# Kernel tuning notes

Measured on AMD Instinct MI355X. Metric: run time of the kernel, lower is better.

The kernel has to match this reference:

```python
import jax, jax.numpy as jnp
import numpy as np

H = 64        # index_n_heads
D = 128       # index_head_dim
R = 64        # rope_head_dim
TOPK = 512    # index_topk
FP8_MAX = 448.0
EPS = 1e-6
THETA = 10000.0


def setup_inputs() -> dict:
    key = jax.random.key(0)
    ks = jax.random.split(key, 6)
    T, DM, QL = 1536, 7168, 1536
    return {
        "hidden_states": jax.random.normal(ks[0], (T, DM), jnp.float32),
        "q_lora": jax.random.normal(ks[1], (T, QL), jnp.float32),
        "wq_b": jax.random.normal(ks[2], (QL, H * D), jnp.float32) / np.sqrt(QL),
        "wk": jax.random.normal(ks[3], (DM, D), jnp.float32) / np.sqrt(DM),
        "k_norm_w": jnp.ones((D,), jnp.float32),
        "k_norm_b": jnp.zeros((D,), jnp.float32),
        "weights_proj_w": jax.random.normal(ks[4], (DM, H), jnp.float32) / np.sqrt(DM),
        "positions": jnp.arange(T, dtype=jnp.int32),
    }


def _rope_neox(x, pos):
    # x: [T, ..., R]; pos: [T]. NEOX-style (half-split) rotary on the rope slice.
    half = R // 2
    inv = 1.0 / (THETA ** (jnp.arange(half, dtype=jnp.float32) / half))
    ang = pos.astype(jnp.float32)[:, None] * inv  # [T, half]
    cos, sin = jnp.cos(ang), jnp.sin(ang)
    while cos.ndim < x.ndim:
        cos, sin = cos[:, None, :], sin[:, None, :]
    x1, x2 = x[..., :half], x[..., half:]
    return jnp.concatenate([x1 * cos - x2 * sin, x2 * cos + x1 * sin], axis=-1)


def _fp8_quant(x):
    # per-row (last-dim) e4m3 quantization: value -> fp8 payload + fp32 scale
    scale = jnp.maximum(jnp.max(jnp.abs(x), axis=-1, keepdims=True) / FP8_MAX, 1e-12)
    xq = (x / scale).astype(jnp.float8_e4m3fn).astype(jnp.float32)
    return xq, scale


def reference(hidden_states, q_lora, wq_b, wk, k_norm_w, k_norm_b, weights_proj_w, positions):
    T = hidden_states.shape[0]
    softmax_scale = D ** (-0.5)
    weights_scale = H ** (-0.5)

    # projections
    q = (q_lora @ wq_b).reshape(T, H, D)          # wq_b
    k = hidden_states @ wk                        # wk

    # k_norm (LayerNorm)
    mu = jnp.mean(k, axis=-1, keepdims=True)
    var = jnp.mean((k - mu) ** 2, axis=-1, keepdims=True)
    k = (k - mu) * jax.lax.rsqrt(var + EPS) * k_norm_w + k_norm_b

    # RoPE on the first rope_head_dim dims of q and k
    q = jnp.concatenate([_rope_neox(q[..., :R], positions), q[..., R:]], axis=-1)
    k = jnp.concatenate([_rope_neox(k[..., :R], positions), k[..., R:]], axis=-1)

    # fp8 quantization (per token-head for q, per token for k)
    q_fp8, q_scale = _fp8_quant(q)   # [T,H,D], [T,H,1]
    k_fp8, k_scale = _fp8_quant(k)   # [T,D],   [T,1]

    # head-gate weights: weights_proj(x) * q_scale * softmax_scale * weights_scale
    gate = hidden_states @ weights_proj_w                      # [T,H]
    w = gate[..., None] * q_scale * (softmax_scale * weights_scale)  # [T,H,1]

    # index score: I[t,s] = sum_h w[t,h] * relu(q[t,h] . k[s]) * k_scale[s]
    qk = jnp.einsum('thd,sd->ths', q_fp8, k_fp8)               # [T,H,S]
    score = jnp.einsum('th,ths->ts', w[..., 0], jax.nn.relu(qk))
    score = score * k_scale[:, 0][None, :]

    # causal (ragged prefill) mask + topk block selection
    causal = positions[:, None] >= positions[None, :]
    score = jnp.where(causal, score, -jnp.inf)
    vals, idx = jax.lax.top_k(score, TOPK)
    idx = jnp.where(jnp.isfinite(vals), idx, -1)
    return idx, vals
```

## Files before the change

### kernel.cpp

```cpp
#include <hip/hip_runtime.h>
#include <hip/hip_bf16.h>
#include <math.h>

#define T_SZ 1536
#define DM_SZ 7168
#define QL_SZ 1536
#define H_SZ 64
#define D_SZ 128
#define ND 8192
#define TOPK_SZ 512
#define N2 192
#define SPLITK2 16

typedef float f32x4 __attribute__((ext_vector_type(4)));
typedef short s16x8 __attribute__((ext_vector_type(8)));
typedef unsigned long long u64;

static __device__ __forceinline__ unsigned char f32_to_e4m3(float x){
  unsigned int b = __float_as_uint(x);
  unsigned int s = (b >> 24) & 0x80u;
  float a = fabsf(x);
  if (a < 0.015625f){
    int m = (int)rintf(a * 512.0f);
    if (m == 8) return (unsigned char)(s | 0x08u);
    return (unsigned char)(s | (unsigned)m);
  }
  int e;
  float mant = frexpf(a, &e);
  int E = e - 1;
  int m = (int)rintf(mant * 16.0f) - 8;
  if (m == 8){ E += 1; m = 0; }
  if (E > 8 || (E == 8 && m > 6)) return (unsigned char)(s | 0x7Eu);
  return (unsigned char)(s | ((unsigned)(E + 7) << 3) | (unsigned)m);
}

static __device__ __forceinline__ unsigned short bf16_rne(float x){
  unsigned int u = __float_as_uint(x);
  return (unsigned short)((u + 0x7FFFu + ((u >> 16) & 1u)) >> 16);
}

typedef __attribute__((address_space(1))) const void gas_void;
typedef __attribute__((address_space(3))) void las_void;
static __device__ __forceinline__ void stage16(const void* g, void* l){
  __builtin_amdgcn_global_load_lds((gas_void*)g, (las_void*)l, 16, 0, 0);
}

__global__ __launch_bounds__(256) void prep_all_k(const float* __restrict__ ql,
                                                  const float* __restrict__ wqb,
                                                  const float* __restrict__ wk,
                                                  const float* __restrict__ wp,
                                                  const int* __restrict__ pos,
                                                  unsigned short* __restrict__ Ahi,
                                                  unsigned short* __restrict__ Alo,
                                                  unsigned short* __restrict__ Bth,
                                                  unsigned short* __restrict__ Btl,
                                                  unsigned short* __restrict__ w2hi,
                                                  unsigned short* __restrict__ w2lo,
                                                  float* __restrict__ cs){
  __shared__ float ld[32][33];
  const int blk = blockIdx.x, tid = threadIdx.x;
  if (blk < 2304){
    int i = blk * 256 + tid;
    float4 v = *(const float4*)&ql[(size_t)i * 4];
    float f[4] = {v.x, v.y, v.z, v.w};
    unsigned short hb[4], lb[4];
#pragma unroll
    for (int j = 0; j < 4; ++j){
      hb[j] = bf16_rne(f[j]);
      float hf = __uint_as_float((unsigned int)hb[j] << 16);
      lb[j] = bf16_rne(f[j] - hf);
    }
    ushort4 h, l;
    h.x = hb[0]; h.y = hb[1]; h.z = hb[2]; h.w = hb[3];
    l.x = lb[0]; l.y = lb[1]; l.z = lb[2]; l.w = lb[3];
    *(ushort4*)&Ahi[(size_t)i * 4] = h;
    *(ushort4*)&Alo[(size_t)i * 4] = l;
  } else if (blk < 14592){
    int f2 = blk - 2304;
    const int n0 = (f2 & 255) * 32, k0 = (f2 >> 8) * 32;
    const int r = tid >> 3, c4 = (tid & 7) * 4;
    float4 v = *(const float4*)&wqb[(size_t)(k0 + r) * ND + n0 + c4];
    ld[r][c4 + 0] = v.x; ld[r][c4 + 1] = v.y; ld[r][c4 + 2] = v.z; ld[r][c4 + 3] = v.w;
    __syncthreads();
    unsigned short hb[4], lb[4];
#pragma unroll
    for (int j = 0; j < 4; ++j){
      float x = ld[c4 + j][r];
      hb[j] = bf16_rne(x);
      float hf = __uint_as_float((unsigned int)hb[j] << 16);
      lb[j] = bf16_rne(x - hf);
    }
    ushort4 h, l;
    h.x = hb[0]; h.y = hb[1]; h.z = hb[2]; h.w = hb[3];
    l.x = lb[0]; l.y = lb[1]; l.z = lb[2]; l.w = lb[3];
    *(ushort4*)&Bth[(size_t)(n0 + r) * QL_SZ + k0 + c4] = h;
    *(ushort4*)&Btl[(size_t)(n0 + r) * QL_SZ + k0 + c4] = l;
  } else if (blk < 15936){
    int g = blk - 14592;
    const int n0 = (g % 6) * 32, k0 = (g / 6) * 32;
    const int r = tid >> 3, c4 = (tid & 7) * 4;
    float4 v;
    if (n0 < 128) v = *(const float4*)&wk[(size_t)(k0 + r) * 128 + n0 + c4];
    else          v = *(const float4*)&wp[(size_t)(k0 + r) * 64 + (n0 - 128) + c4];
    ld[r][c4 + 0] = v.x; ld[r][c4 + 1] = v.y; ld[r][c4 + 2] = v.z; ld[r][c4 + 3] = v.w;
    __syncthreads();
    unsigned short hb[4], lb[4];
#pragma unroll
    for (int j = 0; j < 4; ++j){
      float x = ld[c4 + j][r];
      hb[j] = bf16_rne(x);
      float hf = __uint_as_float((unsigned int)hb[j] << 16);
      lb[j] = bf16_rne(x - hf);
    }
    ushort4 h, l;
    h.x = hb[0]; h.y = hb[1]; h.z = hb[2]; h.w = hb[3];
    l.x = lb[0]; l.y = lb[1]; l.z = lb[2]; l.w = lb[3];
    *(ushort4*)&w2hi[(size_t)(n0 + r) * DM_SZ + k0 + c4] = h;
    *(ushort4*)&w2lo[(size_t)(n0 + r) * DM_SZ + k0 + c4] = l;
  } else {
    int i = (blk - 15936) * 256 + tid;
    int t = i >> 5, j = i & 31;
    float inv = 1.0f / powf(10000.0f, (float)j * (1.0f / 32.0f));
    float ang = (float)pos[t] * inv;
    cs[t * 64 + j]      = cosf(ang);
    cs[t * 64 + 32 + j] = sinf(ang);
  }
}

__global__ void rope_table_k(const int* __restrict__ pos, float* __restrict__ cs){
  int i = blockIdx.x * blockDim.x + threadIdx.x;
  if (i >= T_SZ * 32) return;
  int t = i >> 5, j = i & 31;
  float inv = 1.0f / powf(10000.0f, (float)j * (1.0f / 32.0f));
  float ang = (float)pos[t] * inv;
  cs[t * 64 + j]      = cosf(ang);
  cs[t * 64 + 32 + j] = sinf(ang);
}

__global__ __launch_bounds__(256) void gemm1_mfma_k(const unsigned short* __restrict__ Ahi,
                                                    const unsigned short* __restrict__ Alo,
                                                    const unsigned short* __restrict__ Bhi,
                                                    const unsigned short* __restrict__ Blo,
                                                    float* __restrict__ C){
  __shared__ unsigned short As [128 * 64];
  __shared__ unsigned short Bs0[128 * 64];
  __shared__ unsigned short Bs1[128 * 64];
  const int bid = blockIdx.x;
  const int lid = (bid & 7) * 96 + (bid >> 3);
  const int mt = lid % 12, nt = lid / 12;
  const int m0 = mt * 128, n0 = nt * 128;
  const int tid = threadIdx.x;
  const int w = tid >> 6, l = tid & 63;
  const int wr = w >> 1, wc = w & 1;
  const int lr = l & 15, lg = l >> 4;

  const int srow = w * 32 + (l >> 3);
  const int ssl  = (l & 7) ^ ((l >> 3) & 7);
  const size_t gA = (size_t)(m0 + srow) * QL_SZ + ssl * 8;
  const size_t gB = (size_t)(n0 + srow) * QL_SZ + ssl * 8;
  const int lbase = w * 2048;

  f32x4 acc[4][4];
#pragma unroll
  for (int i = 0; i < 4; ++i)
#pragma unroll
    for (int j = 0; j < 4; ++j) acc[i][j] = (f32x4){0.f, 0.f, 0.f, 0.f};

  const int amrow = wr * 64 + lr;
  const int bnrow = wc * 64 + lr;

  for (int k0 = 0; k0 < QL_SZ; k0 += 64){
#pragma unroll
    for (int i = 0; i < 4; ++i){
      size_t go = (size_t)i * 8 * QL_SZ + k0;
      stage16(Ahi + gA + go, As  + lbase + i * 512);
      stage16(Bhi + gB + go, Bs0 + lbase + i * 512);
      stage16(Blo + gB + go, Bs1 + lbase + i * 512);
    }
    __syncthreads();
#pragma unroll
    for (int kk = 0; kk < 2; ++kk){
      s16x8 af[4], b0[4], b1[4];
#pragma unroll
      for (int f = 0; f < 4; ++f){
        int ma = amrow + f * 16;
        int nb = bnrow + f * 16;
        int sa = ((kk * 4 + lg) ^ (ma & 7)) * 16;
        int sb = ((kk * 4 + lg) ^ (nb & 7)) * 16;
        af[f] = *(const s16x8*)((const char*)As  + ma * 128 + sa);
        b0[f] = *(const s16x8*)((const char*)Bs0 + nb * 128 + sb);
        b1[f] = *(const s16x8*)((const char*)Bs1 + nb * 128 + sb);
      }
#pragma unroll
      for (int fi = 0; fi < 4; ++fi)
#pragma unroll
        for (int fj = 0; fj < 4; ++fj)
          acc[fi][fj] = __builtin_amdgcn_mfma_f32_16x16x32_bf16(af[fi], b0[fj], acc[fi][fj], 0, 0, 0);
#pragma unroll
      for (int fi = 0; fi < 4; ++fi)
#pragma unroll
        for (int fj = 0; fj < 4; ++fj)
          acc[fi][fj] = __builtin_amdgcn_mfma_f32_16x16x32_bf16(af[fi], b1[fj], acc[fi][fj], 0, 0, 0);
    }
    __syncthreads();
#pragma unroll
    for (int i = 0; i < 4; ++i)
      stage16(Alo + gA + (size_t)i * 8 * QL_SZ + k0, As + lbase + i * 512);
    __syncthreads();
#pragma unroll
    for (int kk = 0; kk < 2; ++kk){
      s16x8 af[4], b0[4];
#pragma unroll
      for (int f = 0; f < 4; ++f){
        int ma = amrow + f * 16;
        int nb = bnrow + f * 16;
        af[f] = *(const s16x8*)((const char*)As  + ma * 128 + (((kk * 4 + lg) ^ (ma & 7)) * 16));
        b0[f] = *(const s16x8*)((const char*)Bs0 + nb * 128 + (((kk * 4 + lg) ^ (nb & 7)) * 16));
      }
#pragma unroll
      for (int fi = 0; fi < 4; ++fi)
#pragma unroll
        for (int fj = 0; fj < 4; ++fj)
          acc[fi][fj] = __builtin_amdgcn_mfma_f32_16x16x32_bf16(af[fi], b0[fj], acc[fi][fj], 0, 0, 0);
    }
    __syncthreads();
  }

#pragma unroll
  for (int fi = 0; fi < 4; ++fi){
    const int row = m0 + wr * 64 + fi * 16 + lg * 4;
#pragma unroll
    for (int fj = 0; fj < 4; ++fj){
      float* cp = C + (size_t)row * ND + n0 + wc * 64 + fj * 16 + lr;
      f32x4 d = acc[fi][fj];
      cp[0]              = d.x;
      cp[(size_t)ND]     = d.y;
      cp[(size_t)2 * ND] = d.z;
      cp[(size_t)3 * ND] = d.w;
    }
  }
}

__global__ __launch_bounds__(128) void gemm2_mfma_k(const float* __restrict__ hs,
                                                    const unsigned short* __restrict__ Bhi,
                                                    const unsigned short* __restrict__ Blo,
                                                    float* __restrict__ part){
  __shared__ unsigned short As0[128 * 64];
  __shared__ unsigned short As1[128 * 64];
  __shared__ unsigned short Bs0[64 * 64];
  __shared__ unsigned short Bs1[64 * 64];
  const int bid = blockIdx.x;
  const int lid = (bid & 7) * 72 + (bid >> 3);
  const int s   = lid / 36;
  const int rem = lid % 36;
  const int mt = rem / 3, nt = rem % 3;
  const int m0 = mt * 128, n0 = nt * 64;
  const int kbeg = s * (DM_SZ / SPLITK2);
  const int tid = threadIdx.x;
  const int w = tid >> 6, l = tid & 63;
  const int lr = l & 15, lg = l >> 4;

  const int srow = tid >> 3;
  const int ssl  = (tid & 7) ^ (srow & 7);
  const size_t gB = (size_t)(n0 + srow) * DM_SZ + ssl * 8;
  const int lbase = w * 512;

  f32x4 acc[4][4];
#pragma unroll
  for (int i = 0; i < 4; ++i)
#pragma unroll
    for (int j = 0; j < 4; ++j) acc[i][j] = (f32x4){0.f, 0.f, 0.f, 0.f};

  const int amrow = w * 64 + lr;
  const int bnrow = lr;

  for (int k0 = kbeg; k0 < kbeg + DM_SZ / SPLITK2; k0 += 64){
    f32x4 av[16];
#pragma unroll
    for (int i = 0; i < 8; ++i){
      int idx8 = tid + i * 128;
      int ar = idx8 >> 3, as = idx8 & 7;
      const float* src = hs + (size_t)(m0 + ar) * DM_SZ + k0 + as * 8;
      av[2 * i]     = *(const f32x4*)src;
      av[2 * i + 1] = *(const f32x4*)(src + 4);
    }
#pragma unroll
    for (int i = 0; i < 4; ++i){
      stage16(Bhi + gB + (size_t)i * 16 * DM_SZ + k0, Bs0 + lbase + i * 1024);
      stage16(Blo + gB + (size_t)i * 16 * DM_SZ + k0, Bs1 + lbase + i * 1024);
    }
#pragma unroll
    for (int i = 0; i < 8; ++i){
      int idx8 = tid + i * 128;
      int ar = idx8 >> 3, as = idx8 & 7;
      float f[8];
      *(f32x4*)&f[0] = av[2 * i];
      *(f32x4*)&f[4] = av[2 * i + 1];
      unsigned short hb[8], lb[8];
#pragma unroll
      for (int j = 0; j < 8; ++j){
        hb[j] = bf16_rne(f[j]);
        float hf = __uint_as_float((unsigned int)hb[j] << 16);
        lb[j] = bf16_rne(f[j] - hf);
      }
      int loff = ar * 64 + (as ^ (ar & 7)) * 8;
      *(s16x8*)&As0[loff] = *(s16x8*)hb;
      *(s16x8*)&As1[loff] = *(s16x8*)lb;
    }
    __syncthreads();
#pragma unroll
    for (int kk = 0; kk < 2; ++kk){
      s16x8 ah[4], al[4], b0[4], b1[4];
#pragma unroll
      for (int f = 0; f < 4; ++f){
        int ma = amrow + f * 16;
        int nb = bnrow + f * 16;
        int sa = ((kk * 4 + lg) ^ (ma & 7)) * 16;
        int sb = ((kk * 4 + lg) ^ (nb & 7)) * 16;
        ah[f] = *(const s16x8*)((const char*)As0 + ma * 128 + sa);
        al[f] = *(const s16x8*)((const char*)As1 + ma * 128 + sa);
        b0[f] = *(const s16x8*)((const char*)Bs0 + nb * 128 + sb);
        b1[f] = *(const s16x8*)((const char*)Bs1 + nb * 128 + sb);
      }
#pragma unroll
      for (int fi = 0; fi < 4; ++fi)
#pragma unroll
        for (int fj = 0; fj < 4; ++fj)
          acc[fi][fj] = __builtin_amdgcn_mfma_f32_16x16x32_bf16(ah[fi], b0[fj], acc[fi][fj], 0, 0, 0);
#pragma unroll
      for (int fi = 0; fi < 4; ++fi)
#pragma unroll
        for (int fj = 0; fj < 4; ++fj)
          acc[fi][fj] = __builtin_amdgcn_mfma_f32_16x16x32_bf16(ah[fi], b1[fj], acc[fi][fj], 0, 0, 0);
#pragma unroll
      for (int fi = 0; fi < 4; ++fi)
#pragma unroll
        for (int fj = 0; fj < 4; ++fj)
          acc[fi][fj] = __builtin_amdgcn_mfma_f32_16x16x32_bf16(al[fi], b0[fj], acc[fi][fj], 0, 0, 0);
    }
    __syncthreads();
  }

  float* p = part + (size_t)(s * 36 + mt * 3 + nt) * (128 * 64);
#pragma unroll
  for (int fi = 0; fi < 4; ++fi){
    const int row = w * 64 + fi * 16 + lg * 4;
#pragma unroll
    for (int fj = 0; fj < 4; ++fj){
      float* cp = p + (size_t)row * 64 + fj * 16 + lr;
      f32x4 d = acc[fi][fj];
      cp[  0] = d.x;
      cp[ 64] = d.y;
      cp[128] = d.z;
      cp[192] = d.w;
    }
  }
}

__global__ __launch_bounds__(128) void kpost2_k(const float* __restrict__ part,
                                                const float* __restrict__ knw,
                                                const float* __restrict__ knb,
                                                const float* __restrict__ cs,
                                                unsigned char* __restrict__ kf8,
                                                float* __restrict__ kscale,
                                                float* __restrict__ gate){
  const int t = blockIdx.x, d = threadIdx.x;
  const int mt = t >> 7, rl = t & 127;
  __shared__ float sh[128];
  __shared__ float red[2];
  const float* pk = part + (size_t)(mt * 3 + (d >> 6)) * 8192 + rl * 64 + (d & 63);
  float x = 0.0f;
#pragma unroll
  for (int s = 0; s < SPLITK2; ++s) x += pk[(size_t)s * 36 * 8192];
  if (d < 64){
    const float* pg = part + (size_t)(mt * 3 + 2) * 8192 + rl * 64 + d;
    float gsum = 0.0f;
#pragma unroll
    for (int s = 0; s < SPLITK2; ++s) gsum += pg[(size_t)s * 36 * 8192];
    gate[t * 64 + d] = gsum;
  }
  float v = x;
#pragma unroll
  for (int o = 32; o > 0; o >>= 1) v += __shfl_xor(v, o, 64);
  if ((d & 63) == 0) red[d >> 6] = v;
  __syncthreads();
  float mu = (red[0] + red[1]) / 128.0f;
  float dx = x - mu;
  v = dx * dx;
  __syncthreads();
#pragma unroll
  for (int o = 32; o > 0; o >>= 1) v += __shfl_xor(v, o, 64);
  if ((d & 63) == 0) red[d >> 6] = v;
  __syncthreads();
  float var = (red[0] + red[1]) / 128.0f;
  float nv = dx * (1.0f / sqrtf(var + 1e-6f)) * knw[d] + knb[d];
  sh[d] = nv;
  __syncthreads();
  float outv;
  const float* ct = cs + t * 64;
  if (d < 32)        outv = nv * ct[d] - sh[d + 32] * ct[32 + d];
  else if (d < 64){ int j = d - 32; outv = nv * ct[j] + sh[j] * ct[32 + j]; }
  else               outv = nv;
  v = fabsf(outv);
  __syncthreads();
#pragma unroll
  for (int o = 32; o > 0; o >>= 1) v = fmaxf(v, __shfl_xor(v, o, 64));
  if ((d & 63) == 0) red[d >> 6] = v;
  __syncthreads();
  float amax = fmaxf(red[0], red[1]);
  float scale = fmaxf(amax / 448.0f, 1e-12f);
  kf8[t * 128 + d] = f32_to_e4m3(outv / scale);
  if (d == 0) kscale[t] = scale;
}

__global__ __launch_bounds__(256) void gemm1_k(const float* __restrict__ A,
                                               const float* __restrict__ B,
                                               float* __restrict__ C){
  __shared__ float As[8][132];
  __shared__ float Bs[8][132];
  const int tid = threadIdx.x;
  const int bm = blockIdx.y * 128, bn = blockIdx.x * 128;
  const int ty = tid >> 4, tx = tid & 15;
  const int arow = tid >> 1, ak = (tid & 1) * 4;
  const int brow = tid >> 5, bcol = (tid & 31) * 4;
  float acc[8][8];
#pragma unroll
  for (int i = 0; i < 8; i++)
#pragma unroll
    for (int j = 0; j < 8; j++) acc[i][j] = 0.0f;

  for (int k0 = 0; k0 < QL_SZ; k0 += 8){
    float4 av = *(const float4*)&A[(size_t)(bm + arow) * QL_SZ + k0 + ak];
    float4 bv = *(const float4*)&B[(size_t)(k0 + brow) * ND + bn + bcol];
    As[ak + 0][arow] = av.x; As[ak + 1][arow] = av.y;
    As[ak + 2][arow] = av.z; As[ak + 3][arow] = av.w;
    *(float4*)&Bs[brow][bcol] = bv;
    __syncthreads();
#pragma unroll
    for (int kk = 0; kk < 8; ++kk){
      float a[8], b[8];
      *(float4*)&a[0] = *(const float4*)&As[kk][ty * 8];
      *(float4*)&a[4] = *(const float4*)&As[kk][ty * 8 + 4];
      *(float4*)&b[0] = *(const float4*)&Bs[kk][tx * 8];
      *(float4*)&b[4] = *(const float4*)&Bs[kk][tx * 8 + 4];
#pragma unroll
      for (int i = 0; i < 8; i++)
#pragma unroll
        for (int j = 0; j < 8; j++) acc[i][j] += a[i] * b[j];
    }
    __syncthreads();
  }
#pragma unroll
  for (int i = 0; i < 8; i++)
#pragma unroll
    for (int j = 0; j < 8; j += 4){
      float4 o; o.x = acc[i][j]; o.y = acc[i][j+1]; o.z = acc[i][j+2]; o.w = acc[i][j+3];
      *(float4*)&C[(size_t)(bm + ty * 8 + i) * ND + bn + tx * 8 + j] = o;
    }
}

__global__ __launch_bounds__(256) void gemm2_partial_k(const float* __restrict__ hs,
                                                       const float* __restrict__ wk,
                                                       const float* __restrict__ wp,
                                                       float* __restrict__ part){
  __shared__ float As[32][33];
  __shared__ float Bs[32][196];
  const int tid = threadIdx.x;
  const int m0 = blockIdx.x * 32;
  const int ks = blockIdx.y;
  const int kbeg = ks * (DM_SZ / 8), kend = kbeg + DM_SZ / 8;
  const int arow = tid >> 3, ak4 = (tid & 7) * 4;
  const int r2 = (tid >> 4) * 2, cg = (tid & 15) * 12;
  float acc[2][12];
#pragma unroll
  for (int i = 0; i < 2; i++)
#pragma unroll
    for (int j = 0; j < 12; j++) acc[i][j] = 0.0f;

  for (int k0 = kbeg; k0 < kend; k0 += 32){
    float4 av = *(const float4*)&hs[(size_t)(m0 + arow) * DM_SZ + k0 + ak4];
    As[ak4 + 0][arow] = av.x; As[ak4 + 1][arow] = av.y;
    As[ak4 + 2][arow] = av.z; As[ak4 + 3][arow] = av.w;
#pragma unroll
    for (int i = 0; i < 6; ++i){
      int fi = tid + i * 256;
      int row = fi / 48, c4 = fi % 48;
      float4 bv;
      if (c4 < 32) bv = *(const float4*)&wk[(size_t)(k0 + row) * 128 + c4 * 4];
      else         bv = *(const float4*)&wp[(size_t)(k0 + row) * 64 + (c4 - 32) * 4];
      *(float4*)&Bs[row][c4 * 4] = bv;
    }
    __syncthreads();
#pragma unroll
    for (int kk = 0; kk < 32; ++kk){
      float a0 = As[kk][r2], a1 = As[kk][r2 + 1];
      float b[12];
      *(float4*)&b[0] = *(const float4*)&Bs[kk][cg];
      *(float4*)&b[4] = *(const float4*)&Bs[kk][cg + 4];
      *(float4*)&b[8] = *(const float4*)&Bs[kk][cg + 8];
#pragma unroll
      for (int j = 0; j < 12; j++){ acc[0][j] += a0 * b[j]; acc[1][j] += a1 * b[j]; }
    }
    __syncthreads();
  }
  float* p = part + (size_t)(ks * 48 + blockIdx.x) * 32 * 192;
#pragma unroll
  for (int i = 0; i < 2; i++)
#pragma unroll
    for (int j = 0; j < 12; j += 4){
      float4 o; o.x = acc[i][j]; o.y = acc[i][j+1]; o.z = acc[i][j+2]; o.w = acc[i][j+3];
      *(float4*)&p[(r2 + i) * 192 + cg + j] = o;
    }
}

__global__ void gemm2_reduce_k(const float* __restrict__ part,
                               float* __restrict__ kraw, float* __restrict__ gate){
  int e = blockIdx.x * 256 + threadIdx.x;
  if (e >= T_SZ * 192) return;
  int r = e / 192, c = e % 192;
  int mt = r >> 5, rl = r & 31;
  float s = 0.0f;
  for (int ks = 0; ks < 8; ++ks)
    s += part[((size_t)(ks * 48 + mt) * 32 + rl) * 192 + c];
  if (c < 128) kraw[r * 128 + c] = s;
  else         gate[r * 64 + (c - 128)] = s;
}

__global__ __launch_bounds__(128) void k_post_k(const float* __restrict__ kraw,
                                                const float* __restrict__ knw,
                                                const float* __restrict__ knb,
                                                const float* __restrict__ cs,
                                                unsigned char* __restrict__ kf8,
                                                float* __restrict__ kscale){
  const int t = blockIdx.x, d = threadIdx.x;
  __shared__ float sh[128];
  __shared__ float red[2];
  float x = kraw[t * 128 + d];
  float v = x;
#pragma unroll
  for (int o = 32; o > 0; o >>= 1) v += __shfl_xor(v, o, 64);
  if ((d & 63) == 0) red[d >> 6] = v;
  __syncthreads();
  float mu = (red[0] + red[1]) / 128.0f;
  float dx = x - mu;
  v = dx * dx;
  __syncthreads();
#pragma unroll
  for (int o = 32; o > 0; o >>= 1) v += __shfl_xor(v, o, 64);
  if ((d & 63) == 0) red[d >> 6] = v;
  __syncthreads();
  float var = (red[0] + red[1]) / 128.0f;
  float nv = dx * (1.0f / sqrtf(var + 1e-6f)) * knw[d] + knb[d];
  sh[d] = nv;
  __syncthreads();
  float outv;
  const float* ct = cs + t * 64;
  if (d < 32)        outv = nv * ct[d] - sh[d + 32] * ct[32 + d];
  else if (d < 64){ int j = d - 32; outv = nv * ct[j] + sh[j] * ct[32 + j]; }
  else               outv = nv;
  v = fabsf(outv);
  __syncthreads();
#pragma unroll
  for (int o = 32; o > 0; o >>= 1) v = fmaxf(v, __shfl_xor(v, o, 64));
  if ((d & 63) == 0) red[d >> 6] = v;
  __syncthreads();
  float amax = fmaxf(red[0], red[1]);
  float scale = fmaxf(amax / 448.0f, 1e-12f);
  kf8[t * 128 + d] = f32_to_e4m3(outv / scale);
  if (d == 0) kscale[t] = scale;
}

__global__ __launch_bounds__(256) void q_post2_k(const float* __restrict__ q,
                                                 const float* __restrict__ gate,
                                                 const float* __restrict__ cs,
                                                 unsigned char* __restrict__ qf8,
                                                 float* __restrict__ wbuf){
  const int t = blockIdx.x, tid = threadIdx.x;
  const int h = tid >> 2, g = tid & 3;
  __shared__ float sh[64 * 132];
  const float* qrow = q + (size_t)t * 8192;
#pragma unroll
  for (int i = 0; i < 8; ++i){
    int e4 = tid + i * 256;
    int hh = e4 >> 5, dd = (e4 & 31) * 4;
    float4 v = *(const float4*)&qrow[(size_t)e4 * 4];
    float* dst = &sh[hh * 132 + dd];
    dst[0] = v.x; dst[1] = v.y; dst[2] = v.z; dst[3] = v.w;
  }
  __syncthreads();
  const float* ct = cs + t * 64;
  const float* hq = sh + h * 132;
  float x[32];
#pragma unroll
  for (int j = 0; j < 32; ++j) x[j] = hq[g + 4 * j];
  float vals[32];
  float am = 0.0f;
#pragma unroll
  for (int j = 0; j < 8; ++j){
    int d = g + 4 * j;
    float c = ct[d], s = ct[32 + d];
    float lo = x[j] * c - x[j + 8] * s;
    float hi = x[j + 8] * c + x[j] * s;
    vals[j] = lo; vals[j + 8] = hi;
    am = fmaxf(am, fmaxf(fabsf(lo), fabsf(hi)));
  }
#pragma unroll
  for (int j = 16; j < 32; ++j){ vals[j] = x[j]; am = fmaxf(am, fabsf(x[j])); }
  am = fmaxf(am, __shfl_xor(am, 1, 64));
  am = fmaxf(am, __shfl_xor(am, 2, 64));
  float scale = fmaxf(am / 448.0f, 1e-12f);
  unsigned char* qp = qf8 + (size_t)t * 8192 + h * 128 + g;
#pragma unroll
  for (int j = 0; j < 32; ++j) qp[4 * j] = f32_to_e4m3(vals[j] / scale);
  if (g == 0) wbuf[t * 64 + h] = gate[t * 64 + h] * scale * 0.011048543456039806f;
}

__global__ __launch_bounds__(256) void score_mfma_k(const unsigned char* __restrict__ qf8,
                                                    const unsigned char* __restrict__ kf8,
                                                    const float* __restrict__ wbuf,
                                                    const float* __restrict__ kscale,
                                                    float* __restrict__ score){
  const int bid = blockIdx.x;
  const int p = bid >> 1;
  const int h0 = (bid & 1) * 32;
  int bt = (int)((sqrtf(8.0f * (float)p + 1.0f) - 1.0f) * 0.5f);
  while ((bt + 1) * (bt + 2) / 2 <= p) ++bt;
  while (bt * (bt + 1) / 2 > p) --bt;
  const int bs = p - bt * (bt + 1) / 2;
  const int t0 = bt * 64, s0 = bs * 64;
  const int tid = threadIdx.x;
  const int w  = tid >> 6;
  const int l  = tid & 63;
  const int lr = l & 15;
  const int lg = l >> 4;

  __shared__ float wl[64][68];
#pragma unroll
  for (int i = 0; i < 4; i++){
    int fi = tid + i * 256;
    int row = fi >> 4, c4 = (fi & 15) * 4;
    *(float4*)&wl[row][c4] = *(const float4*)&wbuf[(t0 + row) * 64 + c4];
  }

  u64 b00,b01,b02,b03, b10,b11,b12,b13, b20,b21,b22,b23, b30,b31,b32,b33;
  {
    const unsigned char* kb = kf8 + (size_t)s0 * 128 + 8 * lg;
    const unsigned char* k0r = kb + (size_t)(lr     ) * 128;
    const unsigned char* k1r = kb + (size_t)(lr + 16) * 128;
    const unsigned char* k2r = kb + (size_t)(lr + 32) * 128;
    const unsigned char* k3r = kb + (size_t)(lr + 48) * 128;
    b00=*(const u64*)(k0r+0);  b01=*(const u64*)(k0r+32); b02=*(const u64*)(k0r+64); b03=*(const u64*)(k0r+96);
    b10=*(const u64*)(k1r+0);  b11=*(const u64*)(k1r+32); b12=*(const u64*)(k1r+64); b13=*(const u64*)(k1r+96);
    b20=*(const u64*)(k2r+0);  b21=*(const u64*)(k2r+32); b22=*(const u64*)(k2r+64); b23=*(const u64*)(k2r+96);
    b30=*(const u64*)(k3r+0);  b31=*(const u64*)(k3r+32); b32=*(const u64*)(k3r+64); b33=*(const u64*)(k3r+96);
  }
  __syncthreads();

  const unsigned char* qp = qf8 + (size_t)(t0 + 16 * w + lr) * 8192 + h0 * 128 + 8 * lg;
  u64 a0 = *(const u64*)(qp +  0), a1 = *(const u64*)(qp + 32),
      a2 = *(const u64*)(qp + 64), a3 = *(const u64*)(qp + 96);

  f32x4 acc0 = {0,0,0,0}, acc1 = {0,0,0,0}, acc2 = {0,0,0,0}, acc3 = {0,0,0,0};
  const int wrow = 16 * w + 4 * lg;

  for (int h = 0; h < 32; ++h){
    const unsigned char* qn = qp + ((h + 1) & 31) * 128;
    u64 p0 = *(const u64*)(qn +  0), p1 = *(const u64*)(qn + 32),
        p2 = *(const u64*)(qn + 64), p3 = *(const u64*)(qn + 96);

    f32x4 c0 = {0,0,0,0}, c1 = {0,0,0,0}, c2 = {0,0,0,0}, c3 = {0,0,0,0};
    c0 = __builtin_amdgcn_mfma_f32_16x16x32_fp8_fp8((long)a0, (long)b00, c0, 0, 0, 0);
    c1 = __builtin_amdgcn_mfma_f32_16x16x32_fp8_fp8((long)a0, (long)b10, c1, 0, 0, 0);
    c2 = __builtin_amdgcn_mfma_f32_16x16x32_fp8_fp8((long)a0, (long)b20, c2, 0, 0, 0);
    c3 = __builtin_amdgcn_mfma_f32_16x16x32_fp8_fp8((long)a0, (long)b30, c3, 0, 0, 0);
    c0 = __builtin_amdgcn_mfma_f32_16x16x32_fp8_fp8((long)a1, (long)b01, c0, 0, 0, 0);
    c1 = __builtin_amdgcn_mfma_f32_16x16x32_fp8_fp8((long)a1, (long)b11, c1, 0, 0, 0);
    c2 = __builtin_amdgcn_mfma_f32_16x16x32_fp8_fp8((long)a1, (long)b21, c2, 0, 0, 0);
    c3 = __builtin_amdgcn_mfma_f32_16x16x32_fp8_fp8((long)a1, (long)b31, c3, 0, 0, 0);
    c0 = __builtin_amdgcn_mfma_f32_16x16x32_fp8_fp8((long)a2, (long)b02, c0, 0, 0, 0);
    c1 = __builtin_amdgcn_mfma_f32_16x16x32_fp8_fp8((long)a2, (long)b12, c1, 0, 0, 0);
    c2 = __builtin_amdgcn_mfma_f32_16x16x32_fp8_fp8((long)a2, (long)b22, c2, 0, 0, 0);
    c3 = __builtin_amdgcn_mfma_f32_16x16x32_fp8_fp8((long)a2, (long)b32, c3, 0, 0, 0);
    c0 = __builtin_amdgcn_mfma_f32_16x16x32_fp8_fp8((long)a3, (long)b03, c0, 0, 0, 0);
    c1 = __builtin_amdgcn_mfma_f32_16x16x32_fp8_fp8((long)a3, (long)b13, c1, 0, 0, 0);
    c2 = __builtin_amdgcn_mfma_f32_16x16x32_fp8_fp8((long)a3, (long)b23, c2, 0, 0, 0);
    c3 = __builtin_amdgcn_mfma_f32_16x16x32_fp8_fp8((long)a3, (long)b33, c3, 0, 0, 0);

    float w0 = wl[wrow + 0][h0 + h], w1 = wl[wrow + 1][h0 + h],
          w2 = wl[wrow + 2][h0 + h], w3 = wl[wrow + 3][h0 + h];
    acc0.x += w0 * fmaxf(c0.x, 0.0f); acc0.y += w1 * fmaxf(c0.y, 0.0f);
    acc0.z += w2 * fmaxf(c0.z, 0.0f); acc0.w += w3 * fmaxf(c0.w, 0.0f);
    acc1.x += w0 * fmaxf(c1.x, 0.0f); acc1.y += w1 * fmaxf(c1.y, 0.0f);
    acc1.z += w2 * fmaxf(c1.z, 0.0f); acc1.w += w3 * fmaxf(c1.w, 0.0f);
    acc2.x += w0 * fmaxf(c2.x, 0.0f); acc2.y += w1 * fmaxf(c2.y, 0.0f);
    acc2.z += w2 * fmaxf(c2.z, 0.0f); acc2.w += w3 * fmaxf(c2.w, 0.0f);
    acc3.x += w0 * fmaxf(c3.x, 0.0f); acc3.y += w1 * fmaxf(c3.y, 0.0f);
    acc3.z += w2 * fmaxf(c3.z, 0.0f); acc3.w += w3 * fmaxf(c3.w, 0.0f);

    a0 = p0; a1 = p1; a2 = p2; a3 = p3;
  }

  const int trow = t0 + 16 * w + 4 * lg;
  float ks0 = kscale[s0 + lr], ks1 = kscale[s0 + 16 + lr],
        ks2 = kscale[s0 + 32 + lr], ks3 = kscale[s0 + 48 + lr];
  float* sbase = score + (size_t)(bid & 1) * T_SZ * T_SZ;
  float* sp0 = sbase + (size_t)(trow + 0) * T_SZ + s0 + lr;
  float* sp1 = sbase + (size_t)(trow + 1) * T_SZ + s0 + lr;
  float* sp2 = sbase + (size_t)(trow + 2) * T_SZ + s0 + lr;
  float* sp3 = sbase + (size_t)(trow + 3) * T_SZ + s0 + lr;
  sp0[ 0] = acc0.x * ks0; sp1[ 0] = acc0.y * ks0; sp2[ 0] = acc0.z * ks0; sp3[ 0] = acc0.w * ks0;
  sp0[16] = acc1.x * ks1; sp1[16] = acc1.y * ks1; sp2[16] = acc1.z * ks1; sp3[16] = acc1.w * ks1;
  sp0[32] = acc2.x * ks2; sp1[32] = acc2.y * ks2; sp2[32] = acc2.z * ks2; sp3[32] = acc2.w * ks2;
  sp0[48] = acc3.x * ks3; sp1[48] = acc3.y * ks3; sp2[48] = acc3.z * ks3; sp3[48] = acc3.w * ks3;
}

__global__ __launch_bounds__(256) void topk_sel_k(const float* __restrict__ score,
                                                  float* __restrict__ out){
  const int t = blockIdx.x, tid = threadIdx.x;
  const int n = t + 1;
  __shared__ unsigned int U[2048];
  __shared__ unsigned long long cand[512];
  __shared__ unsigned int hist[256];
  __shared__ unsigned int tix[1536];
  __shared__ unsigned int cnts[2];
  __shared__ unsigned int sel[2];

  const float* s0row = score + (size_t)t * T_SZ;
  const float* s1row = score + (size_t)T_SZ * T_SZ + (size_t)t * T_SZ;
#pragma unroll
  for (int m = 0; m < 8; ++m){
    int j = tid + m * 256;
    unsigned int u = 0u;
    if (j < n){
      float val = s0row[j] + s1row[j];
      unsigned int b = __float_as_uint(val);
      u = (b & 0x80000000u) ? ~b : (b | 0x80000000u);
    }
    U[j] = u;
  }
  if (tid < 2) cnts[tid] = 0u;
  __syncthreads();

  if (n > 512){
    unsigned int prefix = 0u, rem = 512u;
#pragma unroll
    for (int level = 0; level < 4; ++level){
      const int shift = 24 - 8 * level;
      hist[tid] = 0u;
      __syncthreads();
#pragma unroll
      for (int m = 0; m < 8; ++m){
        unsigned int u = U[tid + m * 256];
        bool match = (u != 0u) && (level == 0 || (u >> (shift + 8)) == prefix);
        if (match) atomicAdd(&hist[(u >> shift) & 255u], 1u);
      }
      __syncthreads();
      if (tid < 64){
        unsigned int c0 = hist[tid*4], c1 = hist[tid*4+1], c2 = hist[tid*4+2], c3 = hist[tid*4+3];
        unsigned int loc = c0 + c1 + c2 + c3;
        unsigned int acc = loc;
        for (int off = 1; off < 64; off <<= 1){
          unsigned int v = __shfl_down(acc, off, 64);
          if (tid + off < 64) acc += v;
        }
        unsigned int S3 = acc - loc;
        unsigned int S2 = S3 + c3;
        unsigned int S1 = S2 + c2;
        unsigned int S0 = S1 + c1;
        if (S0 < rem && rem <= S0 + c0){ sel[0] = tid*4 + 0; sel[1] = S0; }
        if (S1 < rem && rem <= S1 + c1){ sel[0] = tid*4 + 1; sel[1] = S1; }
        if (S2 < rem && rem <= S2 + c2){ sel[0] = tid*4 + 2; sel[1] = S2; }
        if (S3 < rem && rem <= S3 + c3){ sel[0] = tid*4 + 3; sel[1] = S3; }
      }
      __syncthreads();
      prefix = (prefix << 8) | sel[0];
      rem -= sel[1];
    }
    const unsigned int u_thr = prefix;

#pragma unroll
    for (int m = 0; m < 8; ++m){
      int j = tid + m * 256;
      unsigned int u = U[j];
      if (u > u_thr){
        unsigned int p = atomicAdd(&cnts[0], 1u);
        cand[p] = ((unsigned long long)u << 32) | (unsigned int)(~(unsigned int)j);
      } else if (u == u_thr){
        unsigned int q = atomicAdd(&cnts[1], 1u);
        tix[q] = (unsigned int)j;
      }
    }
    __syncthreads();
    const unsigned int G = cnts[0], Tt = cnts[1];
    if (Tt == rem){
      for (unsigned int q = tid; q < Tt; q += 256)
        cand[G + q] = ((unsigned long long)u_thr << 32) | (unsigned int)(~tix[q]);
      __syncthreads();
    } else {
      if (tid < 64) hist[tid] = 0u;
      __syncthreads();
      for (unsigned int q = tid; q < Tt; q += 256) atomicAdd(&hist[tix[q] >> 5], 1u);
      __syncthreads();
      if (tid == 0){
        unsigned int cum = 0; unsigned int d = 0;
        for (; d < 64; ++d){ unsigned int c = hist[d]; if (cum + c >= rem) break; cum += c; }
        sel[0] = d; sel[1] = rem - cum;
      }
      __syncthreads();
      const unsigned int dA = sel[0], remA = sel[1];
      if (tid < 32) hist[64 + tid] = 0u;
      __syncthreads();
      for (unsigned int q = tid; q < Tt; q += 256){
        unsigned int j = tix[q];
        if ((j >> 5) == dA) atomicAdd(&hist[64 + (j & 31u)], 1u);
      }
      __syncthreads();
      if (tid == 0){
        unsigned int cum = 0; unsigned int e = 0;
        for (; e < 32; ++e){ unsigned int c = hist[64 + e]; if (cum + c >= remA) break; cum += c; }
        sel[0] = dA * 32 + e;
        cnts[1] = 0u;
      }
      __syncthreads();
      const unsigned int jthr = sel[0];
      for (unsigned int q = tid; q < Tt; q += 256){
        unsigned int j = tix[q];
        if (j <= jthr){
          unsigned int p = atomicAdd(&cnts[1], 1u);
          cand[G + p] = ((unsigned long long)u_thr << 32) | (unsigned int)(~j);
        }
      }
      __syncthreads();
    }
  } else {
    for (int i = tid; i < 512; i += 256){
      unsigned int u = (i < n) ? U[i] : 0u;
      cand[i] = u ? (((unsigned long long)u << 32) | (unsigned int)(~(unsigned int)i)) : 0ull;
    }
    __syncthreads();
  }

  u64 a = cand[2 * tid], b = cand[2 * tid + 1];
#pragma unroll
  for (int k = 2; k <= 512; k <<= 1){
#pragma unroll
    for (int j = k >> 1; j >= 1; j >>= 1){
      if (j >= 128){
        __syncthreads();
        cand[2 * tid] = a; cand[2 * tid + 1] = b;
        __syncthreads();
        int e0 = 2 * tid;
        u64 p0 = cand[e0 ^ j], p1 = cand[(e0 + 1) ^ j];
        bool up  = ((e0 & k) == 0);
        bool low = ((e0 & j) == 0);
        bool mx = (up == low);
        a = mx ? (a > p0 ? a : p0) : (a < p0 ? a : p0);
        b = mx ? (b > p1 ? b : p1) : (b < p1 ? b : p1);
      } else if (j >= 2){
        int d = j >> 1;
        u64 p0 = __shfl_xor(a, d, 64);
        u64 p1 = __shfl_xor(b, d, 64);
        bool up  = (((2 * tid) & k) == 0);
        bool low = ((tid & d) == 0);
        bool mx = (up == low);
        a = mx ? (a > p0 ? a : p0) : (a < p0 ? a : p0);
        b = mx ? (b > p1 ? b : p1) : (b < p1 ? b : p1);
      } else {
        bool up = (((2 * tid) & k) == 0);
        u64 mn = a < b ? a : b, mxv = a < b ? b : a;
        a = up ? mxv : mn;
        b = up ? mn : mxv;
      }
    }
  }

#pragma unroll
  for (int m = 0; m < 2; ++m){
    int i = 2 * tid + m;
    u64 kk = m ? b : a;
    unsigned int u = (unsigned int)(kk >> 32);
    unsigned int bb = (u & 0x80000000u) ? (u & 0x7fffffffu) : ~u;
    float val = __uint_as_float(bb);
    int idx = (int)(~(unsigned int)(kk & 0xffffffffu));
    bool fin = (u != 0u) && (val > -__builtin_huge_valf());
    out[(size_t)t * TOPK_SZ + i] = fin ? (float)idx : -1.0f;
    out[(size_t)T_SZ * TOPK_SZ + (size_t)t * TOPK_SZ + i] = fin ? val : -3.0e38f;
  }
}

extern "C" void kernel_launch(void* const* d_in, const int* in_sizes, int n_in,
                              void* d_out, int out_size, void* d_ws, size_t ws_size,
                              hipStream_t stream){
  const float* hs  = (const float*)d_in[0];
  const float* ql  = (const float*)d_in[1];
  const float* wqb = (const float*)d_in[2];
  const float* wk  = (const float*)d_in[3];
  const float* knw = (const float*)d_in[4];
  const float* knb = (const float*)d_in[5];
  const float* wpj = (const float*)d_in[6];
  const int*   pos = (const int*)d_in[7];
  char* ws = (char*)d_ws;
  size_t off = 0;
  auto alloc = [&](size_t b){ size_t o = off; off += (b + 255) & ~(size_t)255; return o; };
  float* cs     = (float*)(ws + alloc((size_t)T_SZ * 64 * 4));
  float* qbuf   = (float*)(ws + alloc((size_t)T_SZ * ND * 4));
  float* kraw   = (float*)(ws + alloc((size_t)T_SZ * 128 * 4));
  float* gate   = (float*)(ws + alloc((size_t)T_SZ * 64 * 4));
  unsigned char* kf8 = (unsigned char*)(ws + alloc((size_t)T_SZ * 128));
  float* kscale = (float*)(ws + alloc((size_t)T_SZ * 4));
  float* wbuf   = (float*)(ws + alloc((size_t)T_SZ * 64 * 4));
  unsigned short* w2hi = (unsigned short*)(ws + alloc((size_t)N2 * DM_SZ * 2));
  unsigned short* w2lo = (unsigned short*)(ws + alloc((size_t)N2 * DM_SZ * 2));
  const size_t base2 = off;

  size_t o1 = base2;
  auto alloc1 = [&](size_t b){ size_t o = o1; o1 += (b + 255) & ~(size_t)255; return o; };
  unsigned short* Ahi = (unsigned short*)(ws + alloc1((size_t)T_SZ * QL_SZ * 2));
  unsigned short* Alo = (unsigned short*)(ws + alloc1((size_t)T_SZ * QL_SZ * 2));
  unsigned short* Bth = (unsigned short*)(ws + alloc1((size_t)ND * QL_SZ * 2));
  unsigned short* Btl = (unsigned short*)(ws + alloc1((size_t)ND * QL_SZ * 2));

  size_t o2 = base2;
  auto alloc2 = [&](size_t b){ size_t o = o2; o2 += (b + 255) & ~(size_t)255; return o; };
  float* part2 = (float*)(ws + alloc2((size_t)SPLITK2 * 36 * 128 * 64 * 4));
  unsigned char* qf8 = (unsigned char*)(ws + alloc2((size_t)T_SZ * ND));

  const bool fit = (o1 <= ws_size) && (o2 <= ws_size);

  float* part_old = (float*)(ws + base2);
  unsigned char* qf8_fb = (unsigned char*)(ws + base2);
  float* score = qbuf;
  float* out = (float*)d_out;

  if (fit){
    prep_all_k<<<dim3(16128), dim3(256), 0, stream>>>(ql, wqb, wk, wpj, pos,
                                                      Ahi, Alo, Bth, Btl, w2hi, w2lo, cs);
    gemm1_mfma_k<<<dim3(768), dim3(256), 0, stream>>>(Ahi, Alo, Bth, Btl, qbuf);
    gemm2_mfma_k<<<dim3(12 * 3 * SPLITK2), dim3(128), 0, stream>>>(hs, w2hi, w2lo, part2);
    kpost2_k<<<dim3(T_SZ), dim3(128), 0, stream>>>(part2, knw, knb, cs, kf8, kscale, gate);
    q_post2_k<<<dim3(T_SZ), dim3(256), 0, stream>>>(qbuf, gate, cs, qf8, wbuf);
    score_mfma_k<<<dim3(600), dim3(256), 0, stream>>>(qf8, kf8, wbuf, kscale, score);
    topk_sel_k<<<dim3(T_SZ), dim3(256), 0, stream>>>(score, out);
  } else {
    rope_table_k<<<dim3((T_SZ * 32 + 255) / 256), dim3(256), 0, stream>>>(pos, cs);
    gemm2_partial_k<<<dim3(48, 8), dim3(256), 0, stream>>>(hs, wk, wpj, part_old);
    gemm2_reduce_k<<<dim3((T_SZ * 192) / 256), dim3(256), 0, stream>>>(part_old, kraw, gate);
    k_post_k<<<dim3(T_SZ), dim3(128), 0, stream>>>(kraw, knw, knb, cs, kf8, kscale);
    gemm1_k<<<dim3(ND / 128, T_SZ / 128), dim3(256), 0, stream>>>(ql, wqb, qbuf);
    q_post2_k<<<dim3(T_SZ), dim3(256), 0, stream>>>(qbuf, gate, cs, qf8_fb, wbuf);
    score_mfma_k<<<dim3(600), dim3(256), 0, stream>>>(qf8_fb, kf8, wbuf, kscale, score);
    topk_sel_k<<<dim3(T_SZ), dim3(256), 0, stream>>>(score, out);
  }
}
```

Measured before the change: 254.6 us.

## Fuse k post-processing with q rope/quant and aggregate topk atomics per wavefront

Merges the k LayerNorm/RoPE/FP8 kernel and the q RoPE/FP8/gate-weight kernel into one 256-thread kernel per token. The gate sum now stays in shared memory instead of making a global round trip, and one launch is removed. The q row is staged through padded shared memory so each group of four threads handles one head. Separately, the top-k candidate gather replaces per-thread shared atomics with wavefront ballot/popcount aggregation, issuing one atomic per wave. This trades per-thread atomic contention for extra ballots and shuffles, and the fused kernel uses more shared memory, which may lower occupancy.

```diff
diff --git a/kernel.cpp b/kernel.cpp
--- a/kernel.cpp
+++ b/kernel.cpp
@@ -357,32 +357,48 @@
   }
 }
 
-__global__ __launch_bounds__(128) void kpost2_k(const float* __restrict__ part,
-                                                const float* __restrict__ knw,
-                                                const float* __restrict__ knb,
-                                                const float* __restrict__ cs,
-                                                unsigned char* __restrict__ kf8,
-                                                float* __restrict__ kscale,
-                                                float* __restrict__ gate){
-  const int t = blockIdx.x, d = threadIdx.x;
+__global__ __launch_bounds__(256) void kq_post_k(const float* __restrict__ part,
+                                                 const float* __restrict__ knw,
+                                                 const float* __restrict__ knb,
+                                                 const float* __restrict__ cs,
+                                                 const float* __restrict__ q,
+                                                 unsigned char* __restrict__ kf8,
+                                                 float* __restrict__ kscale,
+                                                 unsigned char* __restrict__ qf8,
+                                                 float* __restrict__ wbuf){
+  const int t = blockIdx.x, tid = threadIdx.x;
   const int mt = t >> 7, rl = t & 127;
-  __shared__ float sh[128];
+  __shared__ float shq[64 * 132];
+  __shared__ float shk[128];
   __shared__ float red[2];
-  const float* pk = part + (size_t)(mt * 3 + (d >> 6)) * 8192 + rl * 64 + (d & 63);
+  __shared__ float gsh[64];
+  float4 qv[8];
+  const float* qrow = q + (size_t)t * 8192;
+#pragma unroll
+  for (int i = 0; i < 8; ++i) qv[i] = *(const float4*)&qrow[(size_t)(tid + i * 256) * 4];
   float x = 0.0f;
-#pragma unroll
-  for (int s = 0; s < SPLITK2; ++s) x += pk[(size_t)s * 36 * 8192];
-  if (d < 64){
+  if (tid < 128){
+    const float* pk = part + (size_t)(mt * 3 + (tid >> 6)) * 8192 + rl * 64 + (tid & 63);
+#pragma unroll
+    for (int s = 0; s < SPLITK2; ++s) x += pk[(size_t)s * 36 * 8192];
+  } else if (tid < 192){
+    int d = tid - 128;
     const float* pg = part + (size_t)(mt * 3 + 2) * 8192 + rl * 64 + d;
     float gsum = 0.0f;
 #pragma unroll
     for (int s = 0; s < SPLITK2; ++s) gsum += pg[(size_t)s * 36 * 8192];
-    gate[t * 64 + d] = gsum;
+    gsh[d] = gsum;
+  }
+#pragma unroll
+  for (int i = 0; i < 8; ++i){
+    int e4 = tid + i * 256;
+    float* dst = &shq[(e4 >> 5) * 132 + (e4 & 31) * 4];
+    dst[0] = qv[i].x; dst[1] = qv[i].y; dst[2] = qv[i].z; dst[3] = qv[i].w;
   }
   float v = x;
 #pragma unroll
   for (int o = 32; o > 0; o >>= 1) v += __shfl_xor(v, o, 64);
-  if ((d & 63) == 0) red[d >> 6] = v;
+  if (tid < 128 && (tid & 63) == 0) red[tid >> 6] = v;
   __syncthreads();
   float mu = (red[0] + red[1]) / 128.0f;
   float dx = x - mu;
@@ -390,27 +406,60 @@
   __syncthreads();
 #pragma unroll
   for (int o = 32; o > 0; o >>= 1) v += __shfl_xor(v, o, 64);
-  if ((d & 63) == 0) red[d >> 6] = v;
+  if (tid < 128 && (tid & 63) == 0) red[tid >> 6] = v;
   __syncthreads();
   float var = (red[0] + red[1]) / 128.0f;
-  float nv = dx * (1.0f / sqrtf(var + 1e-6f)) * knw[d] + knb[d];
-  sh[d] = nv;
-  __syncthreads();
-  float outv;
   const float* ct = cs + t * 64;
-  if (d < 32)        outv = nv * ct[d] - sh[d + 32] * ct[32 + d];
-  else if (d < 64){ int j = d - 32; outv = nv * ct[j] + sh[j] * ct[32 + j]; }
-  else               outv = nv;
-  v = fabsf(outv);
+  if (tid < 128){
+    float nv = dx * (1.0f / sqrtf(var + 1e-6f)) * knw[tid] + knb[tid];
+    shk[tid] = nv;
+  }
+  __syncthreads();
+  float outv = 0.0f;
+  if (tid < 128){
+    int d = tid;
+    float nv = shk[d];
+    if (d < 32)        outv = nv * ct[d] - shk[d + 32] * ct[32 + d];
+    else if (d < 64){ int j = d - 32; outv = nv * ct[j] + shk[j] * ct[32 + j]; }
+    else               outv = nv;
+  }
+  v = (tid < 128) ? fabsf(outv) : 0.0f;
   __syncthreads();
 #pragma unroll
   for (int o = 32; o > 0; o >>= 1) v = fmaxf(v, __shfl_xor(v, o, 64));
-  if ((d & 63) == 0) red[d >> 6] = v;
-  __syncthreads();
-  float amax = fmaxf(red[0], red[1]);
-  float scale = fmaxf(amax / 448.0f, 1e-12f);
-  kf8[t * 128 + d] = f32_to_e4m3(outv / scale);
-  if (d == 0) kscale[t] = scale;
+  if (tid < 128 && (tid & 63) == 0) red[tid >> 6] = v;
+  __syncthreads();
+  if (tid < 128){
+    float amax = fmaxf(red[0], red[1]);
+    float scale = fmaxf(amax / 448.0f, 1e-12f);
+    kf8[t * 128 + tid] = f32_to_e4m3(outv / scale);
+    if (tid == 0) kscale[t] = scale;
+  }
+  const int h = tid >> 2, g = tid & 3;
+  const float* hq = shq + h * 132;
+  float xx[32];
+#pragma unroll
+  for (int j = 0; j < 32; ++j) xx[j] = hq[g + 4 * j];
+  float vals[32];
+  float am = 0.0f;
+#pragma unroll
+  for (int j = 0; j < 8; ++j){
+    int d = g + 4 * j;
+    float c = ct[d], s = ct[32 + d];
+    float lo = xx[j] * c - xx[j + 8] * s;
+    float hi = xx[j + 8] * c + xx[j] * s;
+    vals[j] = lo; vals[j + 8] = hi;
+    am = fmaxf(am, fmaxf(fabsf(lo), fabsf(hi)));
+  }
+#pragma unroll
+  for (int j = 16; j < 32; ++j){ vals[j] = xx[j]; am = fmaxf(am, fabsf(xx[j])); }
+  am = fmaxf(am, __shfl_xor(am, 1, 64));
+  am = fmaxf(am, __shfl_xor(am, 2, 64));
+  float qscale = fmaxf(am / 448.0f, 1e-12f);
+  unsigned char* qp = qf8 + (size_t)t * 8192 + h * 128 + g;
+#pragma unroll
+  for (int j = 0; j < 32; ++j) qp[4 * j] = f32_to_e4m3(vals[j] / qscale);
+  if (g == 0) wbuf[t * 64 + h] = gsh[h] * qscale * 0.011048543456039806f;
 }
 
 __global__ __launch_bounds__(256) void gemm1_k(const float* __restrict__ A,
@@ -718,6 +767,7 @@
                                                   float* __restrict__ out){
   const int t = blockIdx.x, tid = threadIdx.x;
   const int n = t + 1;
+  const int lane = tid & 63;
   __shared__ unsigned int U[2048];
   __shared__ unsigned long long cand[512];
   __shared__ unsigned int hist[256];
@@ -778,17 +828,23 @@
     }
     const unsigned int u_thr = prefix;
 
+    const u64 lml = (1ull << lane) - 1ull;
 #pragma unroll
     for (int m = 0; m < 8; ++m){
       int j = tid + m * 256;
       unsigned int u = U[j];
-      if (u > u_thr){
-        unsigned int p = atomicAdd(&cnts[0], 1u);
-        cand[p] = ((unsigned long long)u << 32) | (unsigned int)(~(unsigned int)j);
-      } else if (u == u_thr){
-        unsigned int q = atomicAdd(&cnts[1], 1u);
-        tix[q] = (unsigned int)j;
-      }
+      bool pg = (u > u_thr), pt = (u == u_thr);
+      u64 mg = __ballot(pg), mtk = __ballot(pt);
+      unsigned int bg = 0, bt2 = 0;
+      if (lane == 0){
+        if (mg)  bg  = atomicAdd(&cnts[0], (unsigned int)__popcll(mg));
+        if (mtk) bt2 = atomicAdd(&cnts[1], (unsigned int)__popcll(mtk));
+      }
+      bg  = __shfl(bg, 0, 64);
+      bt2 = __shfl(bt2, 0, 64);
+      if (pg)  cand[bg  + (unsigned int)__popcll(mg  & lml)] =
+                 ((unsigned long long)u << 32) | (unsigned int)(~(unsigned int)j);
+      if (pt)  tix[bt2 + (unsigned int)__popcll(mtk & lml)] = (unsigned int)j;
     }
     __syncthreads();
     const unsigned int G = cnts[0], Tt = cnts[1];
@@ -937,8 +993,7 @@
                                                       Ahi, Alo, Bth, Btl, w2hi, w2lo, cs);
     gemm1_mfma_k<<<dim3(768), dim3(256), 0, stream>>>(Ahi, Alo, Bth, Btl, qbuf);
     gemm2_mfma_k<<<dim3(12 * 3 * SPLITK2), dim3(128), 0, stream>>>(hs, w2hi, w2lo, part2);
-    kpost2_k<<<dim3(T_SZ), dim3(128), 0, stream>>>(part2, knw, knb, cs, kf8, kscale, gate);
-    q_post2_k<<<dim3(T_SZ), dim3(256), 0, stream>>>(qbuf, gate, cs, qf8, wbuf);
+    kq_post_k<<<dim3(T_SZ), dim3(256), 0, stream>>>(part2, knw, knb, cs, qbuf, kf8, kscale, qf8, wbuf);
     score_mfma_k<<<dim3(600), dim3(256), 0, stream>>>(qf8, kf8, wbuf, kscale, score);
     topk_sel_k<<<dim3(T_SZ), dim3(256), 0, stream>>>(score, out);
   } else {
```

New measurement: 253.1 us (median of 3 runs). No clear change (-0.6%).
